# Optimization experiments

Hardware: AMD Instinct MI355X
Metric: run time of the kernel (lower is better)

## Reference

```python
import math
import jax, jax.numpy as jnp
import numpy as np

B, H, W, C = 2, 32, 32, 64
K = 15
G = 4
GC = C // G
K2 = K * K
RED = C // 4
MAX_SIGMA = 0.5


def setup_inputs() -> dict:
    key = jax.random.key(0)
    ks = jax.random.split(key, 32)
    f32 = jnp.float32

    def rn(k, shape, std):
        return (jax.random.normal(k, shape) * std).astype(f32)

    lin = 1.0 / math.sqrt(C)
    inp = {
        'x': jax.random.normal(ks[0], (B, H, W, C), f32),
        'raw_sigma': jnp.asarray(math.log(math.exp(0.3) - 1.0), f32),
        'base_offset_scale': jnp.asarray(0.1, f32),
        # input/output projections (stored [in,out])
        'w_ip': rn(ks[1], (C, C), lin), 'b_ip': jnp.zeros((C,), f32),
        'w_op': rn(ks[2], (C, C), lin), 'b_op': jnp.zeros((C,), f32),
        # dw_conv: depthwise 3x3 (HWIO, I=1) then pointwise 1x1 ([in,out])
        'w_dw': rn(ks[3], (3, 3, 1, C), 1.0 / 3.0), 'b_dw': jnp.zeros((C,), f32),
        'w_pw': rn(ks[4], (C, C), lin), 'b_pw': jnp.zeros((C,), f32),
        # offset / mask heads (original zero-inits; small random to exercise path)
        'w_off': rn(ks[5], (C, G * K2 * 2), 0.01), 'b_off': rn(ks[6], (G * K2 * 2,), 0.01),
        'w_msk': rn(ks[7], (C, G * K2), 0.01), 'b_msk': rn(ks[8], (G * K2,), 0.01),
        # kernel MLP: 2 -> 32 -> 32 -> G*GC
        'w_k1': rn(ks[9], (2, 32), 0.5), 'b_k1': jnp.zeros((32,), f32),
        'w_k2': rn(ks[10], (32, 32), 1.0 / math.sqrt(32)), 'b_k2': jnp.zeros((32,), f32),
        'w_k3': rn(ks[11], (32, G * GC), 1.0 / math.sqrt(32)), 'b_k3': jnp.zeros((G * GC,), f32),
        # SE block
        'w_fc1': rn(ks[12], (C, RED), lin), 'b_fc1': jnp.zeros((RED,), f32),
        'w_fc2': rn(ks[13], (RED, C), 1.0 / math.sqrt(RED)), 'b_fc2': jnp.zeros((C,), f32),
    }
    return inp


def _forward(x, raw_sigma, base_offset_scale, w_ip, b_ip, w_op, b_op, w_dw, b_dw,
             w_pw, b_pw, w_off, b_off, w_msk, b_msk, w_k1, b_k1, w_k2, b_k2,
             w_k3, b_k3, w_fc1, b_fc1, w_fc2, b_fc2):
    Bx, Hx, Wx, Cx = x.shape
    sigma = jnp.clip(jax.nn.softplus(raw_sigma), 1e-3, MAX_SIGMA)
    grid = jnp.linspace(-0.5, 0.5, K)  # [K]

    x_proj = x @ w_ip + b_ip  # [B,H,W,C]

    # depthwise 3x3 (SAME) + SiLU + pointwise 1x1
    y = jax.lax.conv_general_dilated(
        x, w_dw, (1, 1), 'SAME',
        dimension_numbers=('NHWC', 'HWIO', 'NHWC'), feature_group_count=Cx) + b_dw
    x_dw = jax.nn.silu(y) @ w_pw + b_pw  # [B,H,W,C]

    # Gaussian envelope over kernel grid, normalized
    env = jnp.exp(-(grid[:, None] ** 2 + grid[None, :] ** 2) / (2.0 * sigma ** 2))
    env = env / jnp.maximum(env.sum(), 1e-8)
    env_flat = env.reshape(1, 1, 1, 1, K2)

    gh, gw = jnp.meshgrid(grid, grid, indexing='ij')
    pos = jnp.stack([gh.ravel(), gw.ravel()], axis=-1) * 2.0  # [K2,2]
    hkw = jax.nn.silu(pos @ w_k1 + b_k1)
    hkw = jax.nn.silu(hkw @ w_k2 + b_k2)
    kw_raw = hkw @ w_k3 + b_k3  # [K2, G*GC]
    # faithful to torch view quirk: (K,K,G,gc) memory reinterpreted as (G,K2,gc)
    kw = kw_raw.reshape(G, K2, GC).reshape(1, 1, 1, G, K2, GC)

    offsets = (x_dw @ w_off + b_off).reshape(Bx, Hx, Wx, G, K2, 2) * base_offset_scale
    raw_mask = (x_dw @ w_msk + b_msk).reshape(Bx, Hx, Wx, G, K2) * env_flat
    attn = jnp.nan_to_num(jax.nn.softmax(raw_mask, axis=-1))

    # absolute sampling locations
    ref = jnp.linspace(-(K // 2), K // 2, K)
    rh, rw = jnp.meshgrid(ref, ref, indexing='ij')  # [K,K]
    pos_h = jnp.arange(Hx, dtype=x.dtype).reshape(1, Hx, 1, 1, 1)
    pos_w = jnp.arange(Wx, dtype=x.dtype).reshape(1, 1, Wx, 1, 1)
    abs_h = pos_h + rh.ravel().reshape(1, 1, 1, 1, K2) + offsets[..., 0]
    abs_w = pos_w + rw.ravel().reshape(1, 1, 1, 1, K2) + offsets[..., 1]
    ah = jnp.clip(abs_h, 0.0, Hx - 1)
    aw = jnp.clip(abs_w, 0.0, Wx - 1)
    h_f = jnp.clip(jnp.floor(ah).astype(jnp.int32), 0, Hx - 1)
    w_f = jnp.clip(jnp.floor(aw).astype(jnp.int32), 0, Wx - 1)
    h_c = jnp.minimum(h_f + 1, Hx - 1)
    w_c = jnp.minimum(w_f + 1, Wx - 1)
    hw = ah - h_f.astype(x.dtype)
    ww = aw - w_f.astype(x.dtype)
    valid = (~((abs_h < 0) | (abs_h > Hx - 1) | (abs_w < 0) | (abs_w > Wx - 1))).astype(x.dtype)

    xg = x_proj.reshape(Bx, Hx, Wx, G, GC)
    b_idx = jnp.arange(Bx).reshape(Bx, 1, 1, 1, 1)
    g_idx = jnp.arange(G).reshape(1, 1, 1, G, 1)
    v_ff = xg[b_idx, h_f, w_f, g_idx]  # [B,H,W,G,K2,GC]
    v_fc = xg[b_idx, h_f, w_c, g_idx]
    v_cf = xg[b_idx, h_c, w_f, g_idx]
    v_cc = xg[b_idx, h_c, w_c, g_idx]
    sampled = (v_ff * ((1 - hw) * (1 - ww) * valid)[..., None]
               + v_fc * ((1 - hw) * ww * valid)[..., None]
               + v_cf * (hw * (1 - ww) * valid)[..., None]
               + v_cc * (hw * ww * valid)[..., None])
    sampled = sampled * kw
    output = (sampled * attn[..., None]).sum(axis=4).reshape(Bx, Hx, Wx, Cx)

    # SE block (no mask, no bias)
    pooled = output.mean(axis=(1, 2), keepdims=True)
    se = jax.nn.silu(pooled @ w_fc1 + b_fc1) @ w_fc2 + b_fc2
    output = output * jax.nn.sigmoid(se)

    out = output @ w_op + b_op
    offset_reg = (offsets ** 2).mean()
    entropy = -(attn * jnp.log(attn + 1e-8)).sum(axis=-1).mean()
    return out, offset_reg, -entropy


def reference(x, raw_sigma, base_offset_scale, w_ip, b_ip, w_op, b_op, w_dw, b_dw,
              w_pw, b_pw, w_off, b_off, w_msk, b_msk, w_k1, b_k1, w_k2, b_k2,
              w_k3, b_k3, w_fc1, b_fc1, w_fc2, b_fc2):
    return _forward(x, raw_sigma, base_offset_scale, w_ip, b_ip, w_op, b_op,
                    w_dw, b_dw, w_pw, b_pw, w_off, b_off, w_msk, b_msk,
                    w_k1, b_k1, w_k2, b_k2, w_k3, b_k3, w_fc1, b_fc1, w_fc2, b_fc2)
```

## Files before the change

kernel.cpp:

```cpp
#include <hip/hip_runtime.h>
#include <math.h>

#define KK2 225
#define NPIX 2048
#define OFFC 1800
#define MSKC 900

#define WS_KW    0
#define WS_XPROJ 16384
#define WS_XDW   (16384+131072)
#define WS_OUT   (16384+2*131072)
#define WS_POOL  (16384+3*131072)
#define WS_GATE  (WS_POOL+128)
#define WS_ENTP  (WS_GATE+128)
#define WS_OFFP  (WS_ENTP+2048)
#define WS_PART2 (WS_OFFP+512)

__device__ __forceinline__ float silu(float a) { return a / (1.f + __expf(-a)); }

__global__ __launch_bounds__(256) void k_pre(
    const float* __restrict__ x,
    const float* __restrict__ w_ip, const float* __restrict__ b_ip,
    const float* __restrict__ w_dw, const float* __restrict__ b_dw,
    const float* __restrict__ w_pw, const float* __restrict__ b_pw,
    const float* __restrict__ w_k1, const float* __restrict__ b_k1,
    const float* __restrict__ w_k2, const float* __restrict__ b_k2,
    const float* __restrict__ w_k3, const float* __restrict__ b_k3,
    float* __restrict__ ws)
{
  int t = threadIdx.x;
  if (blockIdx.x < 512) {
    int px = t >> 6, c = t & 63;
    int pix = blockIdx.x * 4 + px;
    int b = pix >> 10, h = (pix >> 5) & 31, w = pix & 31;
    __shared__ float xs[4][64], ys[4][64];
    xs[px][c] = x[pix*64 + c];
    float acc = b_dw[c];
    #pragma unroll
    for (int dh = -1; dh <= 1; dh++) {
      int hh = h + dh;
      if (hh < 0 || hh > 31) continue;
      #pragma unroll
      for (int dw2 = -1; dw2 <= 1; dw2++) {
        int wp = w + dw2;
        if (wp < 0 || wp > 31) continue;
        acc += x[(((b*32 + hh)*32 + wp) << 6) + c] * w_dw[((dh+1)*3 + (dw2+1))*64 + c];
      }
    }
    ys[px][c] = silu(acc);
    __syncthreads();
    float p1 = b_ip[c], p2 = b_pw[c];
    #pragma unroll 8
    for (int k = 0; k < 64; k++) {
      p1 += xs[px][k] * w_ip[k*64 + c];
      p2 += ys[px][k] * w_pw[k*64 + c];
    }
    ws[WS_XPROJ + pix*64 + c] = p1;
    ws[WS_XDW   + pix*64 + c] = p2;
  } else {
    __shared__ float h1s[4][32], h2s[4][32];
    int tl = t >> 6, lane = t & 63;
    int tap = (blockIdx.x - 512) * 4 + tl;
    int tapc = min(tap, KK2 - 1);
    int i = tapc / 15, j = tapc % 15;
    float gi = -0.5f + (float)i * (1.0f/14.0f);
    float gj = -0.5f + (float)j * (1.0f/14.0f);
    float p0 = gi * 2.f, p1 = gj * 2.f;
    if (lane < 32) {
      float a = p0 * w_k1[lane] + p1 * w_k1[32 + lane] + b_k1[lane];
      h1s[tl][lane] = silu(a);
    }
    __syncthreads();
    if (lane < 32) {
      float a = b_k2[lane];
      #pragma unroll
      for (int q = 0; q < 32; q++) a += h1s[tl][q] * w_k2[q*32 + lane];
      h2s[tl][lane] = silu(a);
    }
    __syncthreads();
    float a = b_k3[lane];
    #pragma unroll
    for (int q = 0; q < 32; q++) a += h2s[tl][q] * w_k3[q*64 + lane];
    if (tap < KK2) ws[WS_KW + tap*64 + lane] = a;
  }
}

__global__ __launch_bounds__(1024) void k_main(
    const float* __restrict__ raw_sigma,
    const float* __restrict__ base_scale,
    const float* __restrict__ w_off, const float* __restrict__ b_off,
    const float* __restrict__ w_msk, const float* __restrict__ b_msk,
    float* __restrict__ ws)
{
  __shared__ float xdT[256];
  __shared__ float env_s[KK2];
  __shared__ float off_s[4*OFFC];
  __shared__ float msk_s[4*MSKC];
  __shared__ float red_s[16];
  __shared__ float ent_sh[16];
  __shared__ float env_sum;

  int t = threadIdx.x;
  int wv = t >> 6, lane = t & 63;
  int pix0 = blockIdx.x * 4;
  int b = pix0 >> 10;

  float sp = log1pf(__expf(raw_sigma[0]));
  float sigma = fminf(fmaxf(sp, 1e-3f), 0.5f);
  float envv = 0.f;
  if (t < KK2) {
    int i = t / 15, j = t % 15;
    float gi = -0.5f + (float)i * (1.0f/14.0f);
    float gj = -0.5f + (float)j * (1.0f/14.0f);
    envv = __expf(-(gi*gi + gj*gj) / (2.f*sigma*sigma));
  }
  if (t < 256) {
    int px = t >> 6, k = t & 63;
    xdT[k*4 + px] = ws[WS_XDW + (pix0 + px)*64 + k];
  }
  {
    float v = envv;
    #pragma unroll
    for (int m = 32; m > 0; m >>= 1) v += __shfl_xor(v, m);
    if (lane == 0) red_s[wv] = v;
    __syncthreads();
    if (t == 0) {
      float s = 0.f;
      #pragma unroll
      for (int q = 0; q < 16; q++) s += red_s[q];
      env_sum = fmaxf(s, 1e-8f);
    }
    __syncthreads();
    if (t < KK2) env_s[t] = envv / env_sum;
  }

  float b0 = b_off[t];
  float b1 = (t < 776) ? b_off[t + 1024] : b_msk[t - 776];
  int  q2 = min(t + 248, MSKC - 1);
  float b2 = b_msk[q2];
  const float* p0 = w_off + t;
  const float* p1 = (t < 776) ? (w_off + 1024 + t) : (w_msk + (t - 776));
  int s1 = (t < 776) ? OFFC : MSKC;
  const float* p2 = w_msk + q2;
  float4 A0 = make_float4(b0,b0,b0,b0);
  float4 A1 = make_float4(b1,b1,b1,b1);
  float4 A2 = make_float4(b2,b2,b2,b2);
  const float4* xv = (const float4*)xdT;
  #pragma unroll 4
  for (int k = 0; k < 64; k++) {
    float4 xk = xv[k];
    float w0 = *p0, w1 = *p1, w2 = *p2;
    A0.x += xk.x*w0; A0.y += xk.y*w0; A0.z += xk.z*w0; A0.w += xk.w*w0;
    A1.x += xk.x*w1; A1.y += xk.y*w1; A1.z += xk.z*w1; A1.w += xk.w*w1;
    A2.x += xk.x*w2; A2.y += xk.y*w2; A2.z += xk.z*w2; A2.w += xk.w*w2;
    p0 += OFFC; p1 += s1; p2 += MSKC;
  }
  float scale = base_scale[0];
  float offreg = 0.f;
  {
    float v;
    v = A0.x*scale; off_s[0*OFFC + t] = v; offreg += v*v;
    v = A0.y*scale; off_s[1*OFFC + t] = v; offreg += v*v;
    v = A0.z*scale; off_s[2*OFFC + t] = v; offreg += v*v;
    v = A0.w*scale; off_s[3*OFFC + t] = v; offreg += v*v;
    if (t < 776) {
      int o = t + 1024;
      v = A1.x*scale; off_s[0*OFFC + o] = v; offreg += v*v;
      v = A1.y*scale; off_s[1*OFFC + o] = v; offreg += v*v;
      v = A1.z*scale; off_s[2*OFFC + o] = v; offreg += v*v;
      v = A1.w*scale; off_s[3*OFFC + o] = v; offreg += v*v;
    } else {
      int q = t - 776;
      msk_s[0*MSKC + q] = A1.x; msk_s[1*MSKC + q] = A1.y;
      msk_s[2*MSKC + q] = A1.z; msk_s[3*MSKC + q] = A1.w;
    }
    if (t < 652) {
      int q = t + 248;
      msk_s[0*MSKC + q] = A2.x; msk_s[1*MSKC + q] = A2.y;
      msk_s[2*MSKC + q] = A2.z; msk_s[3*MSKC + q] = A2.w;
    }
  }
  {
    #pragma unroll
    for (int m = 32; m > 0; m >>= 1) offreg += __shfl_xor(offreg, m);
    __syncthreads();
    if (lane == 0) red_s[wv] = offreg;
    __syncthreads();
    if (t == 0) {
      float s = 0.f;
      #pragma unroll
      for (int q = 0; q < 16; q++) s += red_s[q];
      ws[WS_OFFP + blockIdx.x] = s;
    }
  }

  {
    int px = wv >> 2, g = wv & 3;
    float v[4];
    float m = -INFINITY;
    #pragma unroll
    for (int kk = 0; kk < 4; kk++) {
      int p = lane + kk*64;
      if (p < KK2) { v[kk] = msk_s[px*MSKC + g*KK2 + p] * env_s[p]; m = fmaxf(m, v[kk]); }
      else v[kk] = -INFINITY;
    }
    #pragma unroll
    for (int s = 32; s > 0; s >>= 1) m = fmaxf(m, __shfl_xor(m, s));
    float sum = 0.f;
    #pragma unroll
    for (int kk = 0; kk < 4; kk++) {
      int p = lane + kk*64;
      if (p < KK2) { v[kk] = __expf(v[kk] - m); sum += v[kk]; }
    }
    #pragma unroll
    for (int s = 32; s > 0; s >>= 1) sum += __shfl_xor(sum, s);
    float inv = 1.f / sum;
    float ent = 0.f;
    #pragma unroll
    for (int kk = 0; kk < 4; kk++) {
      int p = lane + kk*64;
      if (p < KK2) {
        float a = v[kk] * inv;
        msk_s[px*MSKC + g*KK2 + p] = a;
        ent += a * __logf(a + 1e-8f);
      }
    }
    #pragma unroll
    for (int s = 32; s > 0; s >>= 1) ent += __shfl_xor(ent, s);
    if (lane == 0) ent_sh[wv] = ent;
  }
  __syncthreads();
  if (t < 4) ws[WS_ENTP + pix0 + t] =
      ent_sh[t*4] + ent_sh[t*4+1] + ent_sh[t*4+2] + ent_sh[t*4+3];

  const float* xp = ws + WS_XPROJ + (size_t)(b << 10)*64;
  int ts = lane >> 2, cl = lane & 3;
  {
    int px = wv >> 2, g = wv & 3;
    int pix = pix0 + px;
    int h = (pix >> 5) & 31, w = pix & 31;
    int cb = g*16 + cl*4;
    float4 acc = make_float4(0.f, 0.f, 0.f, 0.f);
    for (int p = ts; p < KK2; p += 16) {
      float at = msk_s[px*MSKC + g*KK2 + p];
      float2 o01 = *(const float2*)&off_s[px*OFFC + g*450 + p*2];
      float abs_h = (float)(h + (p/15 - 7)) + o01.x;
      float abs_w = (float)(w + (p%15 - 7)) + o01.y;
      float ah = fminf(fmaxf(abs_h, 0.f), 31.f);
      float aw = fminf(fmaxf(abs_w, 0.f), 31.f);
      int hf = (int)floorf(ah);
      int wf = (int)floorf(aw);
      int hc = min(hf + 1, 31), wc = min(wf + 1, 31);
      float hw_ = ah - (float)hf, ww_ = aw - (float)wf;
      float s = (abs_h < 0.f || abs_h > 31.f || abs_w < 0.f || abs_w > 31.f) ? 0.f : at;
      float w00 = (1.f-hw_)*(1.f-ww_)*s, w01 = (1.f-hw_)*ww_*s;
      float w10 = hw_*(1.f-ww_)*s,       w11 = hw_*ww_*s;
      const float4 vff = *(const float4*)&xp[((hf*32 + wf) << 6) + cb];
      const float4 vfc = *(const float4*)&xp[((hf*32 + wc) << 6) + cb];
      const float4 vcf = *(const float4*)&xp[((hc*32 + wf) << 6) + cb];
      const float4 vcc = *(const float4*)&xp[((hc*32 + wc) << 6) + cb];
      const float4 kwv = *(const float4*)&ws[WS_KW + g*3600 + p*16 + cl*4];
      acc.x += (vff.x*w00 + vfc.x*w01 + vcf.x*w10 + vcc.x*w11) * kwv.x;
      acc.y += (vff.y*w00 + vfc.y*w01 + vcf.y*w10 + vcc.y*w11) * kwv.y;
      acc.z += (vff.z*w00 + vfc.z*w01 + vcf.z*w10 + vcc.z*w11) * kwv.z;
      acc.w += (vff.w*w00 + vfc.w*w01 + vcf.w*w10 + vcc.w*w11) * kwv.w;
    }
    #pragma unroll
    for (int m = 4; m < 64; m <<= 1) {
      acc.x += __shfl_xor(acc.x, m);
      acc.y += __shfl_xor(acc.y, m);
      acc.z += __shfl_xor(acc.z, m);
      acc.w += __shfl_xor(acc.w, m);
    }
    if (lane < 4) *(float4*)&ws[WS_OUT + pix*64 + cb] = acc;
  }
}

__global__ __launch_bounds__(256) void k_red(float* __restrict__ ws, float* __restrict__ d_out)
{
  __shared__ float red[256];
  int t = threadIdx.x, blk = blockIdx.x;
  if (blk < 64) {
    int b = blk >> 5, chunk = blk & 31;
    int c = t & 63, str = t >> 6;
    const float* base = ws + WS_OUT + (size_t)((b*1024 + chunk*32) << 6) + c;
    float s = 0.f;
    #pragma unroll
    for (int i = 0; i < 8; i++) s += base[((str + i*4) << 6)];
    red[t] = s;
    __syncthreads();
    if (t < 64) ws[WS_PART2 + blk*64 + t] =
      red[t] + red[t+64] + red[t+128] + red[t+192];
  } else if (blk == 64) {
    float s = 0.f;
    #pragma unroll
    for (int i = 0; i < 8; i++) s += ws[WS_ENTP + t + i*256];
    #pragma unroll
    for (int m = 32; m > 0; m >>= 1) s += __shfl_xor(s, m);
    if ((t & 63) == 0) red[t >> 6] = s;
    __syncthreads();
    if (t == 0) d_out[NPIX*64 + 1] = (red[0] + red[1] + red[2] + red[3]) * (1.f/8192.f);
  } else {
    float s = 0.f;
    #pragma unroll
    for (int i = 0; i < 2; i++) s += ws[WS_OFFP + t + i*256];
    #pragma unroll
    for (int m = 32; m > 0; m >>= 1) s += __shfl_xor(s, m);
    if ((t & 63) == 0) red[t >> 6] = s;
    __syncthreads();
    if (t == 0) d_out[NPIX*64] = (red[0] + red[1] + red[2] + red[3]) * (1.f/3686400.f);
  }
}

__global__ __launch_bounds__(128) void k_se(
    const float* __restrict__ w_fc1, const float* __restrict__ b_fc1,
    const float* __restrict__ w_fc2, const float* __restrict__ b_fc2,
    float* __restrict__ ws)
{
  __shared__ float pool_s[2][64];
  __shared__ float hsh[2][16];
  int t = threadIdx.x;
  int b = t >> 6, c = t & 63;
  {
    float s = 0.f;
    #pragma unroll
    for (int ch = 0; ch < 32; ch++) s += ws[WS_PART2 + (b*32 + ch)*64 + c];
    pool_s[b][c] = s * (1.f/1024.f);
  }
  __syncthreads();
  if (t < 32) {
    int bb = t >> 4, r = t & 15;
    float a = b_fc1[r];
    #pragma unroll 16
    for (int cc = 0; cc < 64; cc++) a += pool_s[bb][cc] * w_fc1[cc*16 + r];
    hsh[bb][r] = silu(a);
  }
  __syncthreads();
  float a = b_fc2[c];
  #pragma unroll
  for (int r = 0; r < 16; r++) a += hsh[b][r] * w_fc2[r*64 + c];
  ws[WS_GATE + b*64 + c] = 1.f / (1.f + __expf(-a));
}

__global__ __launch_bounds__(256) void k_final(
    const float* __restrict__ w_op, const float* __restrict__ b_op,
    const float* __restrict__ ws, float* __restrict__ d_out)
{
  int t = threadIdx.x;
  int px = t >> 6, c = t & 63;
  int pix = blockIdx.x * 4 + px;
  int b = pix >> 10;
  __shared__ float sc[4][64];
  sc[px][c] = ws[WS_OUT + pix*64 + c] * ws[WS_GATE + b*64 + c];
  __syncthreads();
  float a = b_op[c];
  #pragma unroll 8
  for (int k = 0; k < 64; k++) a += sc[px][k] * w_op[k*64 + c];
  d_out[pix*64 + c] = a;
}

extern "C" void kernel_launch(void* const* d_in, const int* in_sizes, int n_in,
                              void* d_out, int out_size, void* d_ws, size_t ws_size,
                              hipStream_t stream)
{
  const float* x     = (const float*)d_in[0];
  const float* rsig  = (const float*)d_in[1];
  const float* bos   = (const float*)d_in[2];
  const float* w_ip  = (const float*)d_in[3];
  const float* b_ip  = (const float*)d_in[4];
  const float* w_op  = (const float*)d_in[5];
  const float* b_op  = (const float*)d_in[6];
  const float* w_dw  = (const float*)d_in[7];
  const float* b_dw  = (const float*)d_in[8];
  const float* w_pw  = (const float*)d_in[9];
  const float* b_pw  = (const float*)d_in[10];
  const float* w_off = (const float*)d_in[11];
  const float* b_off = (const float*)d_in[12];
  const float* w_msk = (const float*)d_in[13];
  const float* b_msk = (const float*)d_in[14];
  const float* w_k1  = (const float*)d_in[15];
  const float* b_k1  = (const float*)d_in[16];
  const float* w_k2  = (const float*)d_in[17];
  const float* b_k2  = (const float*)d_in[18];
  const float* w_k3  = (const float*)d_in[19];
  const float* b_k3  = (const float*)d_in[20];
  const float* w_fc1 = (const float*)d_in[21];
  const float* b_fc1 = (const float*)d_in[22];
  const float* w_fc2 = (const float*)d_in[23];
  const float* b_fc2 = (const float*)d_in[24];
  float* ws  = (float*)d_ws;
  float* out = (float*)d_out;

  hipLaunchKernelGGL(k_pre, dim3(569), dim3(256), 0, stream,
                     x, w_ip, b_ip, w_dw, b_dw, w_pw, b_pw,
                     w_k1, b_k1, w_k2, b_k2, w_k3, b_k3, ws);
  hipLaunchKernelGGL(k_main, dim3(512), dim3(1024), 0, stream,
                     rsig, bos, w_off, b_off, w_msk, b_msk, ws);
  hipLaunchKernelGGL(k_red, dim3(66), dim3(256), 0, stream, ws, out);
  hipLaunchKernelGGL(k_se, dim3(1), dim3(128), 0, stream,
                     w_fc1, b_fc1, w_fc2, b_fc2, ws);
  hipLaunchKernelGGL(k_final, dim3(512), dim3(256), 0, stream,
                     w_op, b_op, ws, out);
}
```

Before: 56.47 us.

## Compute offset/mask projection with bf16 MFMA using pre-converted transposed weights

Adds a pass in k_pre that converts w_off and w_msk to a transposed bf16 layout in workspace. k_main then computes the 64->2700 offset/mask projection with 16x16x32 bf16 MFMA tiles in place of per-thread fp32 FMA loops, and keeps offsets and masks in shared memory as bf16 to halve LDS use. The aim is to cut the FMA and global weight-load cost of the projection, but only 4 of the 16 MFMA rows hold real pixels, and bf16 offsets and attention lose precision in the bilinear sampling positions.

Result: slower. 60.74 us (+7.6%).

```diff
diff --git a/kernel.cpp b/kernel.cpp
--- a/kernel.cpp
+++ b/kernel.cpp
@@ -5,6 +5,8 @@
 #define NPIX 2048
 #define OFFC 1800
 #define MSKC 900
+#define NCOL 2700
+#define NCOLP 2704
 
 #define WS_KW    0
 #define WS_XPROJ 16384
@@ -15,8 +17,20 @@
 #define WS_ENTP  (WS_GATE+128)
 #define WS_OFFP  (WS_ENTP+2048)
 #define WS_PART2 (WS_OFFP+512)
+#define WS_WB    (WS_PART2+4096)
+
+typedef __attribute__((ext_vector_type(8))) short short8;
+typedef __attribute__((ext_vector_type(4))) float f32x4;
 
 __device__ __forceinline__ float silu(float a) { return a / (1.f + __expf(-a)); }
+__device__ __forceinline__ unsigned short f2bf(float f) {
+  unsigned u = __float_as_uint(f);
+  u += 0x7FFFu + ((u >> 16) & 1u);
+  return (unsigned short)(u >> 16);
+}
+__device__ __forceinline__ float bf2f(unsigned short h) {
+  return __uint_as_float(((unsigned)h) << 16);
+}
 
 __global__ __launch_bounds__(256) void k_pre(
     const float* __restrict__ x,
@@ -26,6 +40,7 @@
     const float* __restrict__ w_k1, const float* __restrict__ b_k1,
     const float* __restrict__ w_k2, const float* __restrict__ b_k2,
     const float* __restrict__ w_k3, const float* __restrict__ b_k3,
+    const float* __restrict__ w_off, const float* __restrict__ w_msk,
     float* __restrict__ ws)
 {
   int t = threadIdx.x;
@@ -57,7 +72,7 @@
     }
     ws[WS_XPROJ + pix*64 + c] = p1;
     ws[WS_XDW   + pix*64 + c] = p2;
-  } else {
+  } else if (blockIdx.x < 569) {
     __shared__ float h1s[4][32], h2s[4][32];
     int tl = t >> 6, lane = t & 63;
     int tap = (blockIdx.x - 512) * 4 + tl;
@@ -82,20 +97,34 @@
     #pragma unroll
     for (int q = 0; q < 32; q++) a += h2s[tl][q] * w_k3[q*64 + lane];
     if (tap < KK2) ws[WS_KW + tap*64 + lane] = a;
+  } else {
+    unsigned short* wb = (unsigned short*)(ws + WS_WB);
+    int cb = blockIdx.x - 569;
+    int col = cb*16 + (t & 15);
+    int kk = (t >> 4) * 4;
+    unsigned short v4[4];
+    #pragma unroll
+    for (int j = 0; j < 4; j++) {
+      int k = kk + j;
+      float v = 0.f;
+      if (col < OFFC)      v = w_off[k*OFFC + col];
+      else if (col < NCOL) v = w_msk[k*MSKC + col - OFFC];
+      v4[j] = f2bf(v);
+    }
+    *(uint2*)&wb[(size_t)col*64 + kk] = *(uint2*)v4;
   }
 }
 
 __global__ __launch_bounds__(1024) void k_main(
     const float* __restrict__ raw_sigma,
     const float* __restrict__ base_scale,
-    const float* __restrict__ w_off, const float* __restrict__ b_off,
-    const float* __restrict__ w_msk, const float* __restrict__ b_msk,
+    const float* __restrict__ b_off, const float* __restrict__ b_msk,
     float* __restrict__ ws)
 {
-  __shared__ float xdT[256];
+  __shared__ unsigned short xbs[16*72];
+  __shared__ unsigned short off_s[4*OFFC];
+  __shared__ unsigned short msk_s[4*MSKC];
   __shared__ float env_s[KK2];
-  __shared__ float off_s[4*OFFC];
-  __shared__ float msk_s[4*MSKC];
   __shared__ float red_s[16];
   __shared__ float ent_sh[16];
   __shared__ float env_sum;
@@ -104,6 +133,7 @@
   int wv = t >> 6, lane = t & 63;
   int pix0 = blockIdx.x * 4;
   int b = pix0 >> 10;
+  const unsigned short* wb = (const unsigned short*)(ws + WS_WB);
 
   float sp = log1pf(__expf(raw_sigma[0]));
   float sigma = fminf(fmaxf(sp, 1e-3f), 0.5f);
@@ -116,7 +146,10 @@
   }
   if (t < 256) {
     int px = t >> 6, k = t & 63;
-    xdT[k*4 + px] = ws[WS_XDW + (pix0 + px)*64 + k];
+    xbs[px*72 + k] = f2bf(ws[WS_XDW + (pix0 + px)*64 + k]);
+  } else {
+    int px = 4 + ((t - 256) >> 6), k = (t - 256) & 63;
+    xbs[px*72 + k] = 0;
   }
   {
     float v = envv;
@@ -134,50 +167,40 @@
     if (t < KK2) env_s[t] = envv / env_sum;
   }
 
-  float b0 = b_off[t];
-  float b1 = (t < 776) ? b_off[t + 1024] : b_msk[t - 776];
-  int  q2 = min(t + 248, MSKC - 1);
-  float b2 = b_msk[q2];
-  const float* p0 = w_off + t;
-  const float* p1 = (t < 776) ? (w_off + 1024 + t) : (w_msk + (t - 776));
-  int s1 = (t < 776) ? OFFC : MSKC;
-  const float* p2 = w_msk + q2;
-  float4 A0 = make_float4(b0,b0,b0,b0);
-  float4 A1 = make_float4(b1,b1,b1,b1);
-  float4 A2 = make_float4(b2,b2,b2,b2);
-  const float4* xv = (const float4*)xdT;
-  #pragma unroll 4
-  for (int k = 0; k < 64; k++) {
-    float4 xk = xv[k];
-    float w0 = *p0, w1 = *p1, w2 = *p2;
-    A0.x += xk.x*w0; A0.y += xk.y*w0; A0.z += xk.z*w0; A0.w += xk.w*w0;
-    A1.x += xk.x*w1; A1.y += xk.y*w1; A1.z += xk.z*w1; A1.w += xk.w*w1;
-    A2.x += xk.x*w2; A2.y += xk.y*w2; A2.z += xk.z*w2; A2.w += xk.w*w2;
-    p0 += OFFC; p1 += s1; p2 += MSKC;
-  }
   float scale = base_scale[0];
   float offreg = 0.f;
-  {
-    float v;
-    v = A0.x*scale; off_s[0*OFFC + t] = v; offreg += v*v;
-    v = A0.y*scale; off_s[1*OFFC + t] = v; offreg += v*v;
-    v = A0.z*scale; off_s[2*OFFC + t] = v; offreg += v*v;
-    v = A0.w*scale; off_s[3*OFFC + t] = v; offreg += v*v;
-    if (t < 776) {
-      int o = t + 1024;
-      v = A1.x*scale; off_s[0*OFFC + o] = v; offreg += v*v;
-      v = A1.y*scale; off_s[1*OFFC + o] = v; offreg += v*v;
-      v = A1.z*scale; off_s[2*OFFC + o] = v; offreg += v*v;
-      v = A1.w*scale; off_s[3*OFFC + o] = v; offreg += v*v;
-    } else {
-      int q = t - 776;
-      msk_s[0*MSKC + q] = A1.x; msk_s[1*MSKC + q] = A1.y;
-      msk_s[2*MSKC + q] = A1.z; msk_s[3*MSKC + q] = A1.w;
-    }
-    if (t < 652) {
-      int q = t + 248;
-      msk_s[0*MSKC + q] = A2.x; msk_s[1*MSKC + q] = A2.y;
-      msk_s[2*MSKC + q] = A2.z; msk_s[3*MSKC + q] = A2.w;
+  int px = lane & 15;
+  int rg = lane >> 4;
+  int k0 = rg * 8;
+  const short8* xb_lo = (const short8*)&xbs[px*72 + k0];
+  const short8* xb_hi = (const short8*)&xbs[px*72 + k0 + 32];
+  short8 bfrag_lo = *xb_lo;
+  short8 bfrag_hi = *xb_hi;
+  for (int tile = wv; tile < 169; tile += 16) {
+    int col0 = tile * 16;
+    int m = col0 + px;
+    const short8 a_lo = *(const short8*)&wb[(size_t)m*64 + k0];
+    const short8 a_hi = *(const short8*)&wb[(size_t)m*64 + k0 + 32];
+    f32x4 acc = {0.f, 0.f, 0.f, 0.f};
+    acc = __builtin_amdgcn_mfma_f32_16x16x32_bf16(a_lo, bfrag_lo, acc, 0, 0, 0);
+    acc = __builtin_amdgcn_mfma_f32_16x16x32_bf16(a_hi, bfrag_hi, acc, 0, 0, 0);
+    int cg = col0 + rg * 4;
+    float4 bias;
+    if (cg < OFFC)      bias = *(const float4*)&b_off[cg];
+    else                bias = *(const float4*)&b_msk[cg - OFFC];
+    if (px < 4) {
+      #pragma unroll
+      for (int r = 0; r < 4; r++) {
+        int col = cg + r;
+        float val = acc[r] + ((const float*)&bias)[r];
+        if (col < OFFC) {
+          float o = val * scale;
+          off_s[px*OFFC + col] = f2bf(o);
+          offreg += o * o;
+        } else if (col < NCOL) {
+          msk_s[px*MSKC + col - OFFC] = f2bf(val);
+        }
+      }
     }
   }
   {
@@ -195,13 +218,13 @@
   }
 
   {
-    int px = wv >> 2, g = wv & 3;
+    int spx = wv >> 2, g = wv & 3;
     float v[4];
     float m = -INFINITY;
     #pragma unroll
     for (int kk = 0; kk < 4; kk++) {
       int p = lane + kk*64;
-      if (p < KK2) { v[kk] = msk_s[px*MSKC + g*KK2 + p] * env_s[p]; m = fmaxf(m, v[kk]); }
+      if (p < KK2) { v[kk] = bf2f(msk_s[spx*MSKC + g*KK2 + p]) * env_s[p]; m = fmaxf(m, v[kk]); }
       else v[kk] = -INFINITY;
     }
     #pragma unroll
@@ -221,7 +244,7 @@
       int p = lane + kk*64;
       if (p < KK2) {
         float a = v[kk] * inv;
-        msk_s[px*MSKC + g*KK2 + p] = a;
+        msk_s[spx*MSKC + g*KK2 + p] = f2bf(a);
         ent += a * __logf(a + 1e-8f);
       }
     }
@@ -236,16 +259,18 @@
   const float* xp = ws + WS_XPROJ + (size_t)(b << 10)*64;
   int ts = lane >> 2, cl = lane & 3;
   {
-    int px = wv >> 2, g = wv & 3;
-    int pix = pix0 + px;
+    int spx = wv >> 2, g = wv & 3;
+    int pix = pix0 + spx;
     int h = (pix >> 5) & 31, w = pix & 31;
     int cb = g*16 + cl*4;
     float4 acc = make_float4(0.f, 0.f, 0.f, 0.f);
     for (int p = ts; p < KK2; p += 16) {
-      float at = msk_s[px*MSKC + g*KK2 + p];
-      float2 o01 = *(const float2*)&off_s[px*OFFC + g*450 + p*2];
-      float abs_h = (float)(h + (p/15 - 7)) + o01.x;
-      float abs_w = (float)(w + (p%15 - 7)) + o01.y;
+      float at = bf2f(msk_s[spx*MSKC + g*KK2 + p]);
+      unsigned op = *(const unsigned*)&off_s[spx*OFFC + g*450 + p*2];
+      float o0 = bf2f((unsigned short)(op & 0xFFFFu));
+      float o1 = bf2f((unsigned short)(op >> 16));
+      float abs_h = (float)(h + (p/15 - 7)) + o0;
+      float abs_w = (float)(w + (p%15 - 7)) + o1;
       float ah = fminf(fmaxf(abs_h, 0.f), 31.f);
       float aw = fminf(fmaxf(abs_w, 0.f), 31.f);
       int hf = (int)floorf(ah);
@@ -391,11 +416,11 @@
   float* ws  = (float*)d_ws;
   float* out = (float*)d_out;
 
-  hipLaunchKernelGGL(k_pre, dim3(569), dim3(256), 0, stream,
+  hipLaunchKernelGGL(k_pre, dim3(738), dim3(256), 0, stream,
                      x, w_ip, b_ip, w_dw, b_dw, w_pw, b_pw,
-                     w_k1, b_k1, w_k2, b_k2, w_k3, b_k3, ws);
+                     w_k1, b_k1, w_k2, b_k2, w_k3, b_k3, w_off, w_msk, ws);
   hipLaunchKernelGGL(k_main, dim3(512), dim3(1024), 0, stream,
-                     rsig, bos, w_off, b_off, w_msk, b_msk, ws);
+                     rsig, bos, b_off, b_msk, ws);
   hipLaunchKernelGGL(k_red, dim3(66), dim3(256), 0, stream, ws, out);
   hipLaunchKernelGGL(k_se, dim3(1), dim3(128), 0, stream,
                      w_fc1, b_fc1, w_fc2, b_fc2, ws);
```
